# Optimization experiments

Measured on AMD Instinct MI355X. Metric: run time of the kernel, lower is better.

The kernel has to match this reference:

```python
import jax, jax.numpy as jnp
import numpy as np

N = 50000       # nodes
E = 800000      # directed edges (before self-loops)
F_IN = 256      # input node features
HID = 64        # hidden_channels
HEADS = 4       # heads of conv1
NEG_SLOPE = 0.2 # PyG GATConv LeakyReLU slope


def setup_inputs() -> dict:
    key = jax.random.key(0)
    ks = jax.random.split(key, 10)
    x = jax.random.normal(ks[0], (N, F_IN), dtype=jnp.float32)
    edge_index = jax.random.randint(ks[1], (2, E), 0, N, dtype=jnp.int32)
    # GATConv params: lin weight [F_in, H*C], att_src/att_dst [H, C], bias
    W1 = jax.random.normal(ks[2], (F_IN, HEADS * HID), jnp.float32) * (1.0 / np.sqrt(F_IN))
    att_src1 = jax.random.normal(ks[3], (HEADS, HID), jnp.float32) * (1.0 / np.sqrt(HID))
    att_dst1 = jax.random.normal(ks[4], (HEADS, HID), jnp.float32) * (1.0 / np.sqrt(HID))
    b1 = jnp.zeros((HEADS * HID,), jnp.float32)
    W2 = jax.random.normal(ks[5], (HEADS * HID, HID), jnp.float32) * (1.0 / np.sqrt(HEADS * HID))
    att_src2 = jax.random.normal(ks[6], (1, HID), jnp.float32) * (1.0 / np.sqrt(HID))
    att_dst2 = jax.random.normal(ks[7], (1, HID), jnp.float32) * (1.0 / np.sqrt(HID))
    b2 = jnp.zeros((HID,), jnp.float32)
    return dict(x=x, edge_index=edge_index, W1=W1, att_src1=att_src1,
                att_dst1=att_dst1, b1=b1, W2=W2, att_src2=att_src2,
                att_dst2=att_dst2, b2=b2)


def gat_layer(x, src, dst, W, a_src, a_dst, bias, heads, ch, concat):
    n = x.shape[0]
    xh = (x @ W).reshape(n, heads, ch)                      # [N,H,C]
    al_s = jnp.einsum('nhc,hc->nh', xh, a_src)              # [N,H]
    al_d = jnp.einsum('nhc,hc->nh', xh, a_dst)
    e = jax.nn.leaky_relu(al_s[src] + al_d[dst], NEG_SLOPE) # [Etot,H]
    # segment softmax over incoming edges of each dst node
    m = jax.ops.segment_max(e, dst, num_segments=n)         # every node has a self-loop
    ex = jnp.exp(e - m[dst])
    den = jax.ops.segment_sum(ex, dst, num_segments=n)
    alpha = ex / (den[dst] + 1e-16)                         # [Etot,H]
    out = jax.ops.segment_sum(alpha[:, :, None] * xh[src], dst, num_segments=n)  # [N,H,C]
    out = out.reshape(n, heads * ch) if concat else out.mean(axis=1)
    return out + bias


def reference(x, edge_index, W1, att_src1, att_dst1, b1, W2, att_src2, att_dst2, b2):
    # GATConv default add_self_loops=True
    loops = jnp.arange(x.shape[0], dtype=edge_index.dtype)
    src = jnp.concatenate([edge_index[0], loops])
    dst = jnp.concatenate([edge_index[1], loops])
    h = jax.nn.elu(gat_layer(x, src, dst, W1, att_src1, att_dst1, b1, HEADS, HID, True))
    # dropout omitted (eval mode)
    out = jax.nn.elu(gat_layer(h, src, dst, W2, att_src2, att_dst2, b2, 1, HID, False))
    return out
```

## Files before the change

kernel.cpp:

```cpp
#include <hip/hip_runtime.h>
#include <math.h>


using short8_t  = __attribute__((ext_vector_type(8))) short;
using half8_t   = __attribute__((ext_vector_type(8))) _Float16;
using f32x4     = __attribute__((ext_vector_type(4))) float;
using ushort4v  = __attribute__((ext_vector_type(4))) unsigned short;
using ushort8v  = __attribute__((ext_vector_type(8))) unsigned short;
using half4     = __attribute__((ext_vector_type(4))) _Float16;

__device__ __forceinline__ float leaky02(float t) { return t > 0.f ? t : 0.2f * t; }
__device__ __forceinline__ float elu1(float t) { return t > 0.f ? t : (__expf(t) - 1.f); }

__device__ __forceinline__ unsigned short bf16_rne(float f) {
  unsigned u = __float_as_uint(f);
  unsigned r = u + 0x7FFFu + ((u >> 16) & 1u);
  return (unsigned short)(r >> 16);
}
__device__ __forceinline__ float bf16_to_f(unsigned short h) {
  return __uint_as_float(((unsigned)h) << 16);
}


__global__ __launch_bounds__(256) void count_kernel(const int* __restrict__ dst,
                                                    int* __restrict__ count, int E) {
  int e = blockIdx.x * blockDim.x + threadIdx.x;
  if (e < E) atomicAdd(&count[dst[e]], 1);
}

__global__ __launch_bounds__(256) void scan1_kernel(const int* __restrict__ count,
                                                    int* __restrict__ locpre,
                                                    int* __restrict__ bsum, int n) {
  __shared__ int sh[256];
  int t = threadIdx.x;
  int node = blockIdx.x * 256 + t;
  int v = (node < n) ? ((count[node] + 4) & ~3) : 0;
  sh[t] = v;
  __syncthreads();
  for (int off = 1; off < 256; off <<= 1) {
    int u = (t >= off) ? sh[t - off] : 0;
    __syncthreads();
    sh[t] += u;
    __syncthreads();
  }
  if (node < n) locpre[node] = sh[t] - v;
  if (t == 255) bsum[blockIdx.x] = sh[255];
}

__global__ __launch_bounds__(256) void scan2_kernel(int* __restrict__ bsum, int nb) {
  __shared__ int sh[256];
  int t = threadIdx.x;
  int v = (t < nb) ? bsum[t] : 0;
  sh[t] = v;
  __syncthreads();
  for (int off = 1; off < 256; off <<= 1) {
    int u = (t >= off) ? sh[t - off] : 0;
    __syncthreads();
    sh[t] += u;
    __syncthreads();
  }
  if (t < nb) bsum[t] = sh[t] - v;
}

__global__ __launch_bounds__(256) void scan3_kernel(const int* __restrict__ count,
                                                    const int* __restrict__ locpre,
                                                    const int* __restrict__ bsum,
                                                    int* __restrict__ offsets,
                                                    int* __restrict__ csr,
                                                    int* __restrict__ cursor,
                                                    float* __restrict__ als1s,
                                                    float* __restrict__ als2s,
                                                    int n) {
  int node = blockIdx.x * 256 + threadIdx.x;
  if (node >= n) return;
  int o = bsum[blockIdx.x] + locpre[node];
  int cnt = count[node];
  int padlen = (cnt + 4) & ~3;
  offsets[node] = o;
  csr[o] = node;
  for (int p = 1 + cnt; p < padlen; ++p) csr[o + p] = n;
  cursor[node] = 0;
  if (node == n - 1) offsets[n] = o + padlen;
  if (node == 0) {
    als1s[0] = -1e30f; als1s[1] = -1e30f; als1s[2] = -1e30f; als1s[3] = -1e30f;
    als2s[0] = -1e30f;
  }
}

__global__ __launch_bounds__(256) void scatter_kernel(const int* __restrict__ src,
                                                      const int* __restrict__ dst,
                                                      const int* __restrict__ offsets,
                                                      int* __restrict__ cursor,
                                                      int* __restrict__ csr, int E) {
  int e = blockIdx.x * blockDim.x + threadIdx.x;
  if (e < E) {
    int d = dst[e];
    int pos = atomicAdd(&cursor[d], 1);
    csr[offsets[d] + 1 + pos] = src[e];
  }
}

__global__ __launch_bounds__(256) void convB_kernel(const float* __restrict__ W,
                                                    unsigned short* __restrict__ Bth,
                                                    unsigned short* __restrict__ Btl, int N) {
  int idx = blockIdx.x * blockDim.x + threadIdx.x;
  if (idx >= N * 64) return;
  int n = idx >> 6;
  int k4 = (idx & 63) * 4;
  ushort4v hi, lo;
#pragma unroll
  for (int i = 0; i < 4; ++i) {
    float w = W[(size_t)(k4 + i) * N + n];
    hi[i] = bf16_rne(w);
    lo[i] = bf16_rne(w - bf16_to_f(hi[i]));
  }
  size_t base = (size_t)n * 256 + k4;
  *(ushort4v*)&Bth[base] = hi;
  *(ushort4v*)&Btl[base] = lo;
}

__global__ __launch_bounds__(256) void convB2_kernel(const float* __restrict__ W,
                                                     _Float16* __restrict__ Bt, int N) {
  int idx = blockIdx.x * blockDim.x + threadIdx.x;
  if (idx >= N * 64) return;
  int n = idx >> 6;
  int k4 = (idx & 63) * 4;
  half4 v;
#pragma unroll
  for (int i = 0; i < 4; ++i) v[i] = (_Float16)W[(size_t)(k4 + i) * N + n];
  *(half4*)&Bt[(size_t)n * 256 + k4] = v;
}

__global__ __launch_bounds__(512) void gemm1_fused(
    const float* __restrict__ Af,
    const unsigned short* __restrict__ Bh, const unsigned short* __restrict__ Bl,
    const float* __restrict__ asrc, const float* __restrict__ adst,
    _Float16* __restrict__ xh, float* __restrict__ als, float* __restrict__ ald, int M) {
  constexpr int BM = 128, BK = 32, KTOT = 256, NW = 256;
  constexpr int MR = 4, NR = 4;
  __shared__ __align__(16) unsigned short lsAh[BM * BK];
  __shared__ __align__(16) unsigned short lsAl[BM * BK];
  __shared__ __align__(16) unsigned short lsBh[NW * BK];
  __shared__ __align__(16) unsigned short lsBl[NW * BK];
  const int tid = threadIdx.x;
  const int lane = tid & 63;
  const int w = tid >> 6;
  const int wr = w >> 2, wc = w & 3;
  const int bm = blockIdx.x * BM;

  f32x4 acc[MR][NR];
#pragma unroll
  for (int i = 0; i < MR; ++i)
#pragma unroll
    for (int j = 0; j < NR; ++j) acc[i][j] = (f32x4){0.f, 0.f, 0.f, 0.f};

  for (int k0 = 0; k0 < KTOT; k0 += BK) {
    {
      int row = tid >> 2, c0 = tid & 3;
      int cs = c0 ^ ((row >> 1) & 3);
      float vv[8];
      if (bm + row < M) {
        float4 v0 = *(const float4*)&Af[(size_t)(bm + row) * 256 + k0 + c0 * 8];
        float4 v1 = *(const float4*)&Af[(size_t)(bm + row) * 256 + k0 + c0 * 8 + 4];
        vv[0] = v0.x; vv[1] = v0.y; vv[2] = v0.z; vv[3] = v0.w;
        vv[4] = v1.x; vv[5] = v1.y; vv[6] = v1.z; vv[7] = v1.w;
      } else {
#pragma unroll
        for (int i = 0; i < 8; ++i) vv[i] = 0.f;
      }
      ushort8v hi, lo;
#pragma unroll
      for (int i = 0; i < 8; ++i) {
        hi[i] = bf16_rne(vv[i]);
        lo[i] = bf16_rne(vv[i] - bf16_to_f(hi[i]));
      }
      *(ushort8v*)&lsAh[row * BK + cs * 8] = hi;
      *(ushort8v*)&lsAl[row * BK + cs * 8] = lo;
    }
#pragma unroll
    for (int rnd = 0; rnd < 2; ++rnd) {
      int id = rnd * 512 + tid;
      int row = id >> 2, c0 = id & 3;
      int cs = c0 ^ ((row >> 1) & 3);
      *(ushort8v*)&lsBh[row * BK + cs * 8] =
          *(const ushort8v*)&Bh[(size_t)row * 256 + k0 + c0 * 8];
      *(ushort8v*)&lsBl[row * BK + cs * 8] =
          *(const ushort8v*)&Bl[(size_t)row * 256 + k0 + c0 * 8];
    }
    __syncthreads();
    short8_t afh[MR], afl[MR];
#pragma unroll
    for (int mr = 0; mr < MR; ++mr) {
      int rr = wr * 64 + mr * 16 + (lane & 15);
      int kc = (lane >> 4) ^ ((rr >> 1) & 3);
      afh[mr] = *(const short8_t*)&lsAh[rr * BK + kc * 8];
      afl[mr] = *(const short8_t*)&lsAl[rr * BK + kc * 8];
    }
#pragma unroll
    for (int nr = 0; nr < NR; ++nr) {
      int rn = wc * 64 + nr * 16 + (lane & 15);
      int kc = (lane >> 4) ^ ((rn >> 1) & 3);
      short8_t bh = *(const short8_t*)&lsBh[rn * BK + kc * 8];
      short8_t bl = *(const short8_t*)&lsBl[rn * BK + kc * 8];
#pragma unroll
      for (int mr = 0; mr < MR; ++mr) {
        acc[mr][nr] = __builtin_amdgcn_mfma_f32_16x16x32_bf16(afh[mr], bh, acc[mr][nr], 0, 0, 0);
        acc[mr][nr] = __builtin_amdgcn_mfma_f32_16x16x32_bf16(afl[mr], bh, acc[mr][nr], 0, 0, 0);
        acc[mr][nr] = __builtin_amdgcn_mfma_f32_16x16x32_bf16(afh[mr], bl, acc[mr][nr], 0, 0, 0);
      }
    }
    __syncthreads();
  }

  float as_[NR], ad_[NR];
#pragma unroll
  for (int nr = 0; nr < NR; ++nr) {
    int c = wc * 64 + nr * 16 + (lane & 15);
    as_[nr] = asrc[c];
    ad_[nr] = adst[c];
  }
#pragma unroll
  for (int mr = 0; mr < MR; ++mr) {
#pragma unroll
    for (int j = 0; j < 4; ++j) {
      int r = bm + wr * 64 + mr * 16 + (lane >> 4) * 4 + j;
      bool ok = r < M;
      float s = 0.f, d = 0.f;
#pragma unroll
      for (int nr = 0; nr < NR; ++nr) {
        float v = acc[mr][nr][j];
        if (ok) xh[(size_t)r * 256 + wc * 64 + nr * 16 + (lane & 15)] = (_Float16)v;
        s += v * as_[nr];
        d += v * ad_[nr];
      }
#pragma unroll
      for (int m = 1; m <= 8; m <<= 1) {
        s += __shfl_xor(s, m);
        d += __shfl_xor(d, m);
      }
      if (ok && (lane & 15) == 0) {
        als[r * 4 + wc] = s;
        ald[r * 4 + wc] = d;
      }
    }
  }
}

__global__ __launch_bounds__(256) void gemm2_fused(
    const _Float16* __restrict__ A,
    const _Float16* __restrict__ Bt,
    const float* __restrict__ asrc, const float* __restrict__ adst,
    _Float16* __restrict__ xh, float* __restrict__ als, float* __restrict__ ald, int M) {
  constexpr int BM = 128, BK = 32, KTOT = 256, NW = 64;
  constexpr int MR = 2, NR = 4;
  __shared__ __align__(16) _Float16 lsA[BM * BK];
  __shared__ __align__(16) _Float16 lsB[NW * BK];
  const int tid = threadIdx.x;
  const int lane = tid & 63;
  const int wr = tid >> 6;
  const int bm = blockIdx.x * BM;

  f32x4 acc[MR][NR];
#pragma unroll
  for (int i = 0; i < MR; ++i)
#pragma unroll
    for (int j = 0; j < NR; ++j) acc[i][j] = (f32x4){0.f, 0.f, 0.f, 0.f};

  for (int k0 = 0; k0 < KTOT; k0 += BK) {
#pragma unroll
    for (int rnd = 0; rnd < 2; ++rnd) {
      int id = rnd * 256 + tid;
      int row = id >> 2, c0 = id & 3;
      int cs = c0 ^ ((row >> 1) & 3);
      *(half8_t*)&lsA[row * BK + cs * 8] =
          *(const half8_t*)&A[(size_t)(bm + row) * 256 + k0 + c0 * 8];
    }
    {
      int row = tid >> 2, c0 = tid & 3;
      int cs = c0 ^ ((row >> 1) & 3);
      *(half8_t*)&lsB[row * BK + cs * 8] =
          *(const half8_t*)&Bt[(size_t)row * 256 + k0 + c0 * 8];
    }
    __syncthreads();
    half8_t af[MR], bf[NR];
#pragma unroll
    for (int mr = 0; mr < MR; ++mr) {
      int rr = wr * 32 + mr * 16 + (lane & 15);
      int kc = (lane >> 4) ^ ((rr >> 1) & 3);
      af[mr] = *(const half8_t*)&lsA[rr * BK + kc * 8];
    }
#pragma unroll
    for (int nr = 0; nr < NR; ++nr) {
      int rn = nr * 16 + (lane & 15);
      int kc = (lane >> 4) ^ ((rn >> 1) & 3);
      bf[nr] = *(const half8_t*)&lsB[rn * BK + kc * 8];
    }
    __syncthreads();
#pragma unroll
    for (int mr = 0; mr < MR; ++mr)
#pragma unroll
      for (int nr = 0; nr < NR; ++nr)
        acc[mr][nr] = __builtin_amdgcn_mfma_f32_16x16x32_f16(af[mr], bf[nr], acc[mr][nr], 0, 0, 0);
  }

  float as_[NR], ad_[NR];
#pragma unroll
  for (int nr = 0; nr < NR; ++nr) {
    int c = nr * 16 + (lane & 15);
    as_[nr] = asrc[c];
    ad_[nr] = adst[c];
  }
#pragma unroll
  for (int mr = 0; mr < MR; ++mr) {
#pragma unroll
    for (int j = 0; j < 4; ++j) {
      int r = bm + wr * 32 + mr * 16 + (lane >> 4) * 4 + j;
      bool ok = r < M;
      float s = 0.f, d = 0.f;
#pragma unroll
      for (int nr = 0; nr < NR; ++nr) {
        float v = acc[mr][nr][j];
        if (ok) xh[(size_t)r * 64 + nr * 16 + (lane & 15)] = (_Float16)v;
        s += v * as_[nr];
        d += v * ad_[nr];
      }
#pragma unroll
      for (int m = 1; m <= 8; m <<= 1) {
        s += __shfl_xor(s, m);
        d += __shfl_xor(d, m);
      }
      if (ok && (lane & 15) == 0) {
        als[r] = s;
        ald[r] = d;
      }
    }
  }
}

__global__ __launch_bounds__(256) void agg1_kernel(const _Float16* __restrict__ xh,
                                                   const float* __restrict__ als,
                                                   const float* __restrict__ ald,
                                                   const int* __restrict__ offsets,
                                                   const int* __restrict__ csr,
                                                   const float* __restrict__ bias,
                                                   _Float16* __restrict__ A2, int n) {
  int node = (blockIdx.x * blockDim.x + threadIdx.x) >> 6;
  int lane = threadIdx.x & 63;
  if (node >= n) return;
  int h = lane >> 4;
  int beg = offsets[node], end = offsets[node + 1];
  float ad = ald[node * 4 + h];
  float den = 0.f;
  float ax = 0.f, ay = 0.f, az = 0.f, aw = 0.f;
  for (int e = beg; e < end; e += 4) {
    int4 s4 = *(const int4*)&csr[e];
    float a0 = als[s4.x * 4 + h], a1 = als[s4.y * 4 + h];
    float a2 = als[s4.z * 4 + h], a3 = als[s4.w * 4 + h];
    half4 x0 = *(const half4*)&xh[(size_t)s4.x * 256 + 4 * lane];
    half4 x1 = *(const half4*)&xh[(size_t)s4.y * 256 + 4 * lane];
    half4 x2 = *(const half4*)&xh[(size_t)s4.z * 256 + 4 * lane];
    half4 x3 = *(const half4*)&xh[(size_t)s4.w * 256 + 4 * lane];
    float e0 = __expf(leaky02(a0 + ad));
    float e1 = __expf(leaky02(a1 + ad));
    float e2 = __expf(leaky02(a2 + ad));
    float e3 = __expf(leaky02(a3 + ad));
    den += (e0 + e1) + (e2 + e3);
    ax += e0 * (float)x0[0] + e1 * (float)x1[0] + e2 * (float)x2[0] + e3 * (float)x3[0];
    ay += e0 * (float)x0[1] + e1 * (float)x1[1] + e2 * (float)x2[1] + e3 * (float)x3[1];
    az += e0 * (float)x0[2] + e1 * (float)x1[2] + e2 * (float)x2[2] + e3 * (float)x3[2];
    aw += e0 * (float)x0[3] + e1 * (float)x1[3] + e2 * (float)x2[3] + e3 * (float)x3[3];
  }
  float inv = 1.f / (den + 1e-16f);
  float4 b = *(const float4*)&bias[4 * lane];
  half4 o;
  o[0] = (_Float16)elu1(ax * inv + b.x);
  o[1] = (_Float16)elu1(ay * inv + b.y);
  o[2] = (_Float16)elu1(az * inv + b.z);
  o[3] = (_Float16)elu1(aw * inv + b.w);
  *(half4*)&A2[(size_t)node * 256 + 4 * lane] = o;
}

__global__ __launch_bounds__(256) void agg2_kernel(const _Float16* __restrict__ xh,
                                                   const float* __restrict__ als,
                                                   const float* __restrict__ ald,
                                                   const int* __restrict__ offsets,
                                                   const int* __restrict__ csr,
                                                   const float* __restrict__ bias,
                                                   float* __restrict__ out, int n) {
  int node = (blockIdx.x * blockDim.x + threadIdx.x) >> 6;
  int lane = threadIdx.x & 63;
  if (node >= n) return;
  int g = lane >> 4, li = lane & 15;
  int beg = offsets[node], end = offsets[node + 1];
  float ad = ald[node];
  float den = 0.f;
  float ax = 0.f, ay = 0.f, az = 0.f, aw = 0.f;
  for (int e0 = beg; e0 < end; e0 += 4) {
    int s = csr[e0 + g];
    float ex = __expf(leaky02(als[s] + ad));
    half4 xv = *(const half4*)&xh[(size_t)s * 64 + 4 * li];
    den += ex;
    ax += ex * (float)xv[0]; ay += ex * (float)xv[1];
    az += ex * (float)xv[2]; aw += ex * (float)xv[3];
  }
#pragma unroll
  for (int m = 16; m <= 32; m <<= 1) {
    den += __shfl_xor(den, m);
    ax += __shfl_xor(ax, m);
    ay += __shfl_xor(ay, m);
    az += __shfl_xor(az, m);
    aw += __shfl_xor(aw, m);
  }
  if (g == 0) {
    float inv = 1.f / (den + 1e-16f);
    float4 b = *(const float4*)&bias[4 * li];
    float4 o;
    o.x = elu1(ax * inv + b.x);
    o.y = elu1(ay * inv + b.y);
    o.z = elu1(az * inv + b.z);
    o.w = elu1(aw * inv + b.w);
    *(float4*)&out[(size_t)node * 64 + 4 * li] = o;
  }
}


extern "C" void kernel_launch(void* const* d_in, const int* in_sizes, int n_in,
                              void* d_out, int out_size, void* d_ws, size_t ws_size,
                              hipStream_t stream) {
  const float* x   = (const float*)d_in[0];
  const int*   ei  = (const int*)d_in[1];
  const float* W1  = (const float*)d_in[2];
  const float* as1 = (const float*)d_in[3];
  const float* ad1 = (const float*)d_in[4];
  const float* b1  = (const float*)d_in[5];
  const float* W2  = (const float*)d_in[6];
  const float* as2 = (const float*)d_in[7];
  const float* ad2 = (const float*)d_in[8];
  const float* b2  = (const float*)d_in[9];
  float* out = (float*)d_out;

  const int E = in_sizes[1] / 2;
  const int n = in_sizes[0] / 256;
  const int Mpad = ((n + 127) / 128) * 128;
  const int nb = (n + 255) / 256;

  size_t off = 0;
  auto alloc = [&](size_t bytes) -> void* {
    void* p = (char*)d_ws + off;
    off += (bytes + 511) & ~(size_t)511;
    return p;
  };
  _Float16* xh  = (_Float16*)alloc((size_t)(n + 1) * 256 * 2);
  _Float16* A2  = (_Float16*)alloc((size_t)Mpad * 256 * 2);
  unsigned short* Bh1 = (unsigned short*)alloc((size_t)256 * 256 * 2);
  unsigned short* Bl1 = (unsigned short*)alloc((size_t)256 * 256 * 2);
  _Float16* Bt2 = (_Float16*)alloc((size_t)64 * 256 * 2);
  float* als1v = (float*)alloc((size_t)(n + 1) * 4 * 4);
  float* ald1v = (float*)alloc((size_t)n * 4 * 4);
  float* als2v = (float*)alloc((size_t)(n + 1) * 4);
  float* ald2v = (float*)alloc((size_t)n * 4);
  int* count   = (int*)alloc((size_t)n * 4);
  int* cursor  = (int*)alloc((size_t)n * 4);
  int* offsets = (int*)alloc((size_t)(n + 1) * 4);
  int* locpre  = (int*)alloc((size_t)n * 4);
  int* bsum    = (int*)alloc(256 * 4);
  int* csr     = (int*)alloc((size_t)(E + 4 * n) * 4);

  const int* srcv = ei;
  const int* dstv = ei + E;

  hipMemsetAsync(count, 0, (size_t)n * 4, stream);
  count_kernel<<<(E + 255) / 256, 256, 0, stream>>>(dstv, count, E);
  scan1_kernel<<<nb, 256, 0, stream>>>(count, locpre, bsum, n);
  scan2_kernel<<<1, 256, 0, stream>>>(bsum, nb);
  scan3_kernel<<<nb, 256, 0, stream>>>(count, locpre, bsum, offsets, csr, cursor,
                                       als1v + (size_t)n * 4, als2v + n, n);
  scatter_kernel<<<(E + 255) / 256, 256, 0, stream>>>(srcv, dstv, offsets, cursor, csr, E);

  convB_kernel<<<(256 * 64 + 255) / 256, 256, 0, stream>>>(W1, Bh1, Bl1, 256);
  convB2_kernel<<<(64 * 64 + 255) / 256, 256, 0, stream>>>(W2, Bt2, 64);

  gemm1_fused<<<Mpad / 128, 512, 0, stream>>>(x, Bh1, Bl1, as1, ad1, xh, als1v, ald1v, n);
  agg1_kernel<<<(n + 3) / 4, 256, 0, stream>>>(xh, als1v, ald1v, offsets, csr, b1, A2, n);

  gemm2_fused<<<Mpad / 128, 256, 0, stream>>>(A2, Bt2, as2, ad2, xh, als2v, ald2v, n);
  agg2_kernel<<<(n + 3) / 4, 256, 0, stream>>>(xh, als2v, ald2v, offsets, csr, b2, out, n);
}
```

Before: 338.8 us.

## Use single fp16 MFMA for layer-1 GEMM, fuse small kernels, unroll aggregation loops

Replaces the three-pass split-bf16 MFMA emulation of fp32 in the first GEMM with a single fp16 MFMA pass, which cuts matrix math, LDS traffic and conversion work by about a factor of three. The block-prefix scan is folded into scan3 and the two weight conversion kernels are merged, removing two launches. Both aggregation kernels now process 8 edges per iteration to expose more memory-level parallelism. The fp16 input rounding lowers GEMM accuracy compared with the bf16 hi/lo scheme.

```diff
diff --git a/kernel.cpp b/kernel.cpp
--- a/kernel.cpp
+++ b/kernel.cpp
@@ -2,24 +2,12 @@
 #include <math.h>
 
 
-using short8_t  = __attribute__((ext_vector_type(8))) short;
 using half8_t   = __attribute__((ext_vector_type(8))) _Float16;
 using f32x4     = __attribute__((ext_vector_type(4))) float;
-using ushort4v  = __attribute__((ext_vector_type(4))) unsigned short;
-using ushort8v  = __attribute__((ext_vector_type(8))) unsigned short;
 using half4     = __attribute__((ext_vector_type(4))) _Float16;
 
 __device__ __forceinline__ float leaky02(float t) { return t > 0.f ? t : 0.2f * t; }
 __device__ __forceinline__ float elu1(float t) { return t > 0.f ? t : (__expf(t) - 1.f); }
-
-__device__ __forceinline__ unsigned short bf16_rne(float f) {
-  unsigned u = __float_as_uint(f);
-  unsigned r = u + 0x7FFFu + ((u >> 16) & 1u);
-  return (unsigned short)(r >> 16);
-}
-__device__ __forceinline__ float bf16_to_f(unsigned short h) {
-  return __uint_as_float(((unsigned)h) << 16);
-}
 
 
 __global__ __launch_bounds__(256) void count_kernel(const int* __restrict__ dst,
@@ -47,21 +35,6 @@
   if (t == 255) bsum[blockIdx.x] = sh[255];
 }
 
-__global__ __launch_bounds__(256) void scan2_kernel(int* __restrict__ bsum, int nb) {
-  __shared__ int sh[256];
-  int t = threadIdx.x;
-  int v = (t < nb) ? bsum[t] : 0;
-  sh[t] = v;
-  __syncthreads();
-  for (int off = 1; off < 256; off <<= 1) {
-    int u = (t >= off) ? sh[t - off] : 0;
-    __syncthreads();
-    sh[t] += u;
-    __syncthreads();
-  }
-  if (t < nb) bsum[t] = sh[t] - v;
-}
-
 __global__ __launch_bounds__(256) void scan3_kernel(const int* __restrict__ count,
                                                     const int* __restrict__ locpre,
                                                     const int* __restrict__ bsum,
@@ -70,10 +43,22 @@
                                                     int* __restrict__ cursor,
                                                     float* __restrict__ als1s,
                                                     float* __restrict__ als2s,
-                                                    int n) {
-  int node = blockIdx.x * 256 + threadIdx.x;
+                                                    int n, int nb) {
+  __shared__ int sh[256];
+  int t = threadIdx.x;
+  int v = (t < nb) ? bsum[t] : 0;
+  sh[t] = v;
+  __syncthreads();
+  for (int off = 1; off < 256; off <<= 1) {
+    int u = (t >= off) ? sh[t - off] : 0;
+    __syncthreads();
+    sh[t] += u;
+    __syncthreads();
+  }
+  int bpre = (blockIdx.x == 0) ? 0 : sh[blockIdx.x - 1];
+  int node = blockIdx.x * 256 + t;
   if (node >= n) return;
-  int o = bsum[blockIdx.x] + locpre[node];
+  int o = bpre + locpre[node];
   int cnt = count[node];
   int padlen = (cnt + 4) & ~3;
   offsets[node] = o;
@@ -100,48 +85,38 @@
   }
 }
 
-__global__ __launch_bounds__(256) void convB_kernel(const float* __restrict__ W,
-                                                    unsigned short* __restrict__ Bth,
-                                                    unsigned short* __restrict__ Btl, int N) {
+__global__ __launch_bounds__(256) void convW_kernel(const float* __restrict__ W1,
+                                                    const float* __restrict__ W2,
+                                                    _Float16* __restrict__ Bt1,
+                                                    _Float16* __restrict__ Bt2) {
   int idx = blockIdx.x * blockDim.x + threadIdx.x;
-  if (idx >= N * 64) return;
-  int n = idx >> 6;
-  int k4 = (idx & 63) * 4;
-  ushort4v hi, lo;
-#pragma unroll
-  for (int i = 0; i < 4; ++i) {
-    float w = W[(size_t)(k4 + i) * N + n];
-    hi[i] = bf16_rne(w);
-    lo[i] = bf16_rne(w - bf16_to_f(hi[i]));
-  }
-  size_t base = (size_t)n * 256 + k4;
-  *(ushort4v*)&Bth[base] = hi;
-  *(ushort4v*)&Btl[base] = lo;
-}
-
-__global__ __launch_bounds__(256) void convB2_kernel(const float* __restrict__ W,
-                                                     _Float16* __restrict__ Bt, int N) {
-  int idx = blockIdx.x * blockDim.x + threadIdx.x;
-  if (idx >= N * 64) return;
-  int n = idx >> 6;
-  int k4 = (idx & 63) * 4;
-  half4 v;
-#pragma unroll
-  for (int i = 0; i < 4; ++i) v[i] = (_Float16)W[(size_t)(k4 + i) * N + n];
-  *(half4*)&Bt[(size_t)n * 256 + k4] = v;
+  if (idx < 256 * 64) {
+    int c = idx >> 6;
+    int k4 = (idx & 63) * 4;
+    half4 v;
+#pragma unroll
+    for (int i = 0; i < 4; ++i) v[i] = (_Float16)W1[(size_t)(k4 + i) * 256 + c];
+    *(half4*)&Bt1[(size_t)c * 256 + k4] = v;
+  } else if (idx < 256 * 64 + 64 * 64) {
+    int j = idx - 256 * 64;
+    int c = j >> 6;
+    int k4 = (j & 63) * 4;
+    half4 v;
+#pragma unroll
+    for (int i = 0; i < 4; ++i) v[i] = (_Float16)W2[(size_t)(k4 + i) * 64 + c];
+    *(half4*)&Bt2[(size_t)c * 256 + k4] = v;
+  }
 }
 
 __global__ __launch_bounds__(512) void gemm1_fused(
     const float* __restrict__ Af,
-    const unsigned short* __restrict__ Bh, const unsigned short* __restrict__ Bl,
+    const _Float16* __restrict__ Bt,
     const float* __restrict__ asrc, const float* __restrict__ adst,
     _Float16* __restrict__ xh, float* __restrict__ als, float* __restrict__ ald, int M) {
   constexpr int BM = 128, BK = 32, KTOT = 256, NW = 256;
   constexpr int MR = 4, NR = 4;
-  __shared__ __align__(16) unsigned short lsAh[BM * BK];
-  __shared__ __align__(16) unsigned short lsAl[BM * BK];
-  __shared__ __align__(16) unsigned short lsBh[NW * BK];
-  __shared__ __align__(16) unsigned short lsBl[NW * BK];
+  __shared__ __align__(16) _Float16 lsA[BM * BK];
+  __shared__ __align__(16) _Float16 lsB[NW * BK];
   const int tid = threadIdx.x;
   const int lane = tid & 63;
   const int w = tid >> 6;
@@ -158,57 +133,47 @@
     {
       int row = tid >> 2, c0 = tid & 3;
       int cs = c0 ^ ((row >> 1) & 3);
-      float vv[8];
+      half8_t hv;
       if (bm + row < M) {
         float4 v0 = *(const float4*)&Af[(size_t)(bm + row) * 256 + k0 + c0 * 8];
         float4 v1 = *(const float4*)&Af[(size_t)(bm + row) * 256 + k0 + c0 * 8 + 4];
-        vv[0] = v0.x; vv[1] = v0.y; vv[2] = v0.z; vv[3] = v0.w;
-        vv[4] = v1.x; vv[5] = v1.y; vv[6] = v1.z; vv[7] = v1.w;
+        hv[0] = (_Float16)v0.x; hv[1] = (_Float16)v0.y;
+        hv[2] = (_Float16)v0.z; hv[3] = (_Float16)v0.w;
+        hv[4] = (_Float16)v1.x; hv[5] = (_Float16)v1.y;
+        hv[6] = (_Float16)v1.z; hv[7] = (_Float16)v1.w;
       } else {
 #pragma unroll
-        for (int i = 0; i < 8; ++i) vv[i] = 0.f;
-      }
-      ushort8v hi, lo;
-#pragma unroll
-      for (int i = 0; i < 8; ++i) {
-        hi[i] = bf16_rne(vv[i]);
-        lo[i] = bf16_rne(vv[i] - bf16_to_f(hi[i]));
-      }
-      *(ushort8v*)&lsAh[row * BK + cs * 8] = hi;
-      *(ushort8v*)&lsAl[row * BK + cs * 8] = lo;
+        for (int i = 0; i < 8; ++i) hv[i] = (_Float16)0.f;
+      }
+      *(half8_t*)&lsA[row * BK + cs * 8] = hv;
     }
 #pragma unroll
     for (int rnd = 0; rnd < 2; ++rnd) {
       int id = rnd * 512 + tid;
       int row = id >> 2, c0 = id & 3;
       int cs = c0 ^ ((row >> 1) & 3);
-      *(ushort8v*)&lsBh[row * BK + cs * 8] =
-          *(const ushort8v*)&Bh[(size_t)row * 256 + k0 + c0 * 8];
-      *(ushort8v*)&lsBl[row * BK + cs * 8] =
-          *(const ushort8v*)&Bl[(size_t)row * 256 + k0 + c0 * 8];
-    }
-    __syncthreads();
-    short8_t afh[MR], afl[MR];
+      *(half8_t*)&lsB[row * BK + cs * 8] =
+          *(const half8_t*)&Bt[(size_t)row * 256 + k0 + c0 * 8];
+    }
+    __syncthreads();
+    half8_t af[MR], bf[NR];
 #pragma unroll
     for (int mr = 0; mr < MR; ++mr) {
       int rr = wr * 64 + mr * 16 + (lane & 15);
       int kc = (lane >> 4) ^ ((rr >> 1) & 3);
-      afh[mr] = *(const short8_t*)&lsAh[rr * BK + kc * 8];
-      afl[mr] = *(const short8_t*)&lsAl[rr * BK + kc * 8];
+      af[mr] = *(const half8_t*)&lsA[rr * BK + kc * 8];
     }
 #pragma unroll
     for (int nr = 0; nr < NR; ++nr) {
       int rn = wc * 64 + nr * 16 + (lane & 15);
       int kc = (lane >> 4) ^ ((rn >> 1) & 3);
-      short8_t bh = *(const short8_t*)&lsBh[rn * BK + kc * 8];
-      short8_t bl = *(const short8_t*)&lsBl[rn * BK + kc * 8];
-#pragma unroll
-      for (int mr = 0; mr < MR; ++mr) {
-        acc[mr][nr] = __builtin_amdgcn_mfma_f32_16x16x32_bf16(afh[mr], bh, acc[mr][nr], 0, 0, 0);
-        acc[mr][nr] = __builtin_amdgcn_mfma_f32_16x16x32_bf16(afl[mr], bh, acc[mr][nr], 0, 0, 0);
-        acc[mr][nr] = __builtin_amdgcn_mfma_f32_16x16x32_bf16(afh[mr], bl, acc[mr][nr], 0, 0, 0);
-      }
-    }
+      bf[nr] = *(const half8_t*)&lsB[rn * BK + kc * 8];
+    }
+#pragma unroll
+    for (int mr = 0; mr < MR; ++mr)
+#pragma unroll
+      for (int nr = 0; nr < NR; ++nr)
+        acc[mr][nr] = __builtin_amdgcn_mfma_f32_16x16x32_f16(af[mr], bf[nr], acc[mr][nr], 0, 0, 0);
     __syncthreads();
   }
 
@@ -352,7 +317,41 @@
   float ad = ald[node * 4 + h];
   float den = 0.f;
   float ax = 0.f, ay = 0.f, az = 0.f, aw = 0.f;
-  for (int e = beg; e < end; e += 4) {
+  int e = beg;
+  for (; e + 8 <= end; e += 8) {
+    int4 sa = *(const int4*)&csr[e];
+    int4 sb = *(const int4*)&csr[e + 4];
+    float a0 = als[sa.x * 4 + h], a1 = als[sa.y * 4 + h];
+    float a2 = als[sa.z * 4 + h], a3 = als[sa.w * 4 + h];
+    float a4 = als[sb.x * 4 + h], a5 = als[sb.y * 4 + h];
+    float a6 = als[sb.z * 4 + h], a7 = als[sb.w * 4 + h];
+    half4 x0 = *(const half4*)&xh[(size_t)sa.x * 256 + 4 * lane];
+    half4 x1 = *(const half4*)&xh[(size_t)sa.y * 256 + 4 * lane];
+    half4 x2 = *(const half4*)&xh[(size_t)sa.z * 256 + 4 * lane];
+    half4 x3 = *(const half4*)&xh[(size_t)sa.w * 256 + 4 * lane];
+    half4 x4 = *(const half4*)&xh[(size_t)sb.x * 256 + 4 * lane];
+    half4 x5 = *(const half4*)&xh[(size_t)sb.y * 256 + 4 * lane];
+    half4 x6 = *(const half4*)&xh[(size_t)sb.z * 256 + 4 * lane];
+    half4 x7 = *(const half4*)&xh[(size_t)sb.w * 256 + 4 * lane];
+    float e0 = __expf(leaky02(a0 + ad));
+    float e1 = __expf(leaky02(a1 + ad));
+    float e2 = __expf(leaky02(a2 + ad));
+    float e3 = __expf(leaky02(a3 + ad));
+    float e4 = __expf(leaky02(a4 + ad));
+    float e5 = __expf(leaky02(a5 + ad));
+    float e6 = __expf(leaky02(a6 + ad));
+    float e7 = __expf(leaky02(a7 + ad));
+    den += ((e0 + e1) + (e2 + e3)) + ((e4 + e5) + (e6 + e7));
+    ax += e0 * (float)x0[0] + e1 * (float)x1[0] + e2 * (float)x2[0] + e3 * (float)x3[0]
+        + e4 * (float)x4[0] + e5 * (float)x5[0] + e6 * (float)x6[0] + e7 * (float)x7[0];
+    ay += e0 * (float)x0[1] + e1 * (float)x1[1] + e2 * (float)x2[1] + e3 * (float)x3[1]
+        + e4 * (float)x4[1] + e5 * (float)x5[1] + e6 * (float)x6[1] + e7 * (float)x7[1];
+    az += e0 * (float)x0[2] + e1 * (float)x1[2] + e2 * (float)x2[2] + e3 * (float)x3[2]
+        + e4 * (float)x4[2] + e5 * (float)x5[2] + e6 * (float)x6[2] + e7 * (float)x7[2];
+    aw += e0 * (float)x0[3] + e1 * (float)x1[3] + e2 * (float)x2[3] + e3 * (float)x3[3]
+        + e4 * (float)x4[3] + e5 * (float)x5[3] + e6 * (float)x6[3] + e7 * (float)x7[3];
+  }
+  if (e < end) {
     int4 s4 = *(const int4*)&csr[e];
     float a0 = als[s4.x * 4 + h], a1 = als[s4.y * 4 + h];
     float a2 = als[s4.z * 4 + h], a3 = als[s4.w * 4 + h];
@@ -395,13 +394,27 @@
   float ad = ald[node];
   float den = 0.f;
   float ax = 0.f, ay = 0.f, az = 0.f, aw = 0.f;
-  for (int e0 = beg; e0 < end; e0 += 4) {
+  int e0 = beg;
+  for (; e0 + 8 <= end; e0 += 8) {
+    int s0 = csr[e0 + g];
+    int s1 = csr[e0 + 4 + g];
+    half4 xv0 = *(const half4*)&xh[(size_t)s0 * 64 + 4 * li];
+    half4 xv1 = *(const half4*)&xh[(size_t)s1 * 64 + 4 * li];
+    float w0 = __expf(leaky02(als[s0] + ad));
+    float w1 = __expf(leaky02(als[s1] + ad));
+    den += w0 + w1;
+    ax += w0 * (float)xv0[0] + w1 * (float)xv1[0];
+    ay += w0 * (float)xv0[1] + w1 * (float)xv1[1];
+    az += w0 * (float)xv0[2] + w1 * (float)xv1[2];
+    aw += w0 * (float)xv0[3] + w1 * (float)xv1[3];
+  }
+  if (e0 < end) {
     int s = csr[e0 + g];
-    float ex = __expf(leaky02(als[s] + ad));
     half4 xv = *(const half4*)&xh[(size_t)s * 64 + 4 * li];
-    den += ex;
-    ax += ex * (float)xv[0]; ay += ex * (float)xv[1];
-    az += ex * (float)xv[2]; aw += ex * (float)xv[3];
+    float w = __expf(leaky02(als[s] + ad));
+    den += w;
+    ax += w * (float)xv[0]; ay += w * (float)xv[1];
+    az += w * (float)xv[2]; aw += w * (float)xv[3];
   }
 #pragma unroll
   for (int m = 16; m <= 32; m <<= 1) {
@@ -452,8 +465,7 @@
   };
   _Float16* xh  = (_Float16*)alloc((size_t)(n + 1) * 256 * 2);
   _Float16* A2  = (_Float16*)alloc((size_t)Mpad * 256 * 2);
-  unsigned short* Bh1 = (unsigned short*)alloc((size_t)256 * 256 * 2);
-  unsigned short* Bl1 = (unsigned short*)alloc((size_t)256 * 256 * 2);
+  _Float16* Bt1 = (_Float16*)alloc((size_t)256 * 256 * 2);
   _Float16* Bt2 = (_Float16*)alloc((size_t)64 * 256 * 2);
   float* als1v = (float*)alloc((size_t)(n + 1) * 4 * 4);
   float* ald1v = (float*)alloc((size_t)n * 4 * 4);
@@ -472,15 +484,13 @@
   hipMemsetAsync(count, 0, (size_t)n * 4, stream);
   count_kernel<<<(E + 255) / 256, 256, 0, stream>>>(dstv, count, E);
   scan1_kernel<<<nb, 256, 0, stream>>>(count, locpre, bsum, n);
-  scan2_kernel<<<1, 256, 0, stream>>>(bsum, nb);
   scan3_kernel<<<nb, 256, 0, stream>>>(count, locpre, bsum, offsets, csr, cursor,
-                                       als1v + (size_t)n * 4, als2v + n, n);
+                                       als1v + (size_t)n * 4, als2v + n, n, nb);
   scatter_kernel<<<(E + 255) / 256, 256, 0, stream>>>(srcv, dstv, offsets, cursor, csr, E);
 
-  convB_kernel<<<(256 * 64 + 255) / 256, 256, 0, stream>>>(W1, Bh1, Bl1, 256);
-  convB2_kernel<<<(64 * 64 + 255) / 256, 256, 0, stream>>>(W2, Bt2, 64);
-
-  gemm1_fused<<<Mpad / 128, 512, 0, stream>>>(x, Bh1, Bl1, as1, ad1, xh, als1v, ald1v, n);
+  convW_kernel<<<(256 * 64 + 64 * 64 + 255) / 256, 256, 0, stream>>>(W1, W2, Bt1, Bt2);
+
+  gemm1_fused<<<Mpad / 128, 512, 0, stream>>>(x, Bt1, as1, ad1, xh, als1v, ald1v, n);
   agg1_kernel<<<(n + 3) / 4, 256, 0, stream>>>(xh, als1v, ald1v, offsets, csr, b1, A2, n);
 
   gemm2_fused<<<Mpad / 128, 256, 0, stream>>>(A2, Bt2, as2, ad2, xh, als2v, ald2v, n);
```

New measurement: 310.7 us. 8.3% less time.
